# Kernel tuning notes

Hardware: AMD Instinct MI355X
Metric: run time of the kernel (lower is better)

## Reference

```python
import jax, jax.numpy as jnp
import numpy as np

VOCAB = 100000
EMBED = 64
SENT = 20
MEM = 50
BATCH = 32
HOPS = 3
PAD_ID = 0


def position_encoding(sentence_size, embedding_size):
    # Section 4.1 of MemN2N paper, vectorized. Returns [sentence_size, embedding_size].
    i = np.arange(1, embedding_size + 1, dtype=np.float32)[:, None]   # [E,1]
    j = np.arange(1, sentence_size + 1, dtype=np.float32)[None, :]    # [1,S]
    enc = (i - (embedding_size + 1) / 2.0) * (j - (sentence_size + 1) / 2.0)
    enc = 1.0 + 4.0 * enc / embedding_size / sentence_size
    enc[:, -1] = 1.0
    return jnp.asarray(enc.T, dtype=jnp.float32)  # [S,E]


def setup_inputs() -> dict:
    key = jax.random.key(0)
    k1, k2, k3, k4 = jax.random.split(key, 4)
    stories = jax.random.randint(k1, (BATCH, MEM, SENT), 0, VOCAB, dtype=jnp.int64 if jax.config.jax_enable_x64 else jnp.int32)
    queries = jax.random.randint(k2, (BATCH, SENT), 0, VOCAB, dtype=jnp.int64 if jax.config.jax_enable_x64 else jnp.int32)
    A = jax.random.normal(k3, (VOCAB, EMBED), dtype=jnp.float32) * 0.1
    C = jax.random.normal(k4, (HOPS, VOCAB, EMBED), dtype=jnp.float32) * 0.1
    # padding_idx=PAD_ID rows are zero, as in nn.Embedding(padding_idx=...)
    A = A.at[PAD_ID].set(0.0)
    C = C.at[:, PAD_ID].set(0.0)
    encoding = position_encoding(SENT, EMBED)
    return {"stories": stories, "queries": queries, "A": A, "C": C, "encoding": encoding}


def reference(stories, queries, A, C, encoding):
    # queries: [B,S], stories: [B,M,S], A: [V,E], C: [hops,V,E], encoding: [S,E]
    q_emb = A[queries]                                # [B,S,E]
    u = (q_emb * encoding).sum(axis=1)                # [B,E]
    for hop in range(HOPS):
        table_in = A if hop == 0 else C[hop - 1]
        emb_A = table_in[stories]                     # [B,M,S,E]
        m = (emb_A * encoding).sum(axis=2)            # [B,M,E]
        dotted = jnp.einsum('bme,be->bm', m, u)       # [B,M]
        probs = jax.nn.softmax(dotted, axis=-1)       # [B,M]
        emb_C = C[hop][stories]                       # [B,M,S,E]
        c = (emb_C * encoding).sum(axis=2)            # [B,M,E]
        o = jnp.einsum('bm,bme->be', probs, c)        # [B,E]
        u = u + o
    return u @ C[-1].T                                # [B,V]
```

## Files before the change

kernel.cpp:

```cpp
#include <hip/hip_runtime.h>
#include <hip/hip_bf16.h>

#define VOCAB 100000
#define EMBED 64
#define SENT  20
#define MEM   50
#define BATCH 32
#define HOPS  3

__device__ __forceinline__ float bfr(unsigned short x) {
    union { unsigned int u; float f; } cv;
    cv.u = ((unsigned int)x) << 16;
    return cv.f;
}

__device__ __forceinline__ bool is_bf16(const void* enc) {
    return ((const unsigned int*)enc)[639] == 0x3F803F80u;
}

__device__ __forceinline__ float loadT(const void* p, size_t idx, bool bf) {
    return bf ? bfr(((const unsigned short*)p)[idx]) : ((const float*)p)[idx];
}

__global__ void k_query(const int* __restrict__ queries,
                        const void* __restrict__ A,
                        const void* __restrict__ enc,
                        float* __restrict__ u)
{
    bool bf = is_bf16(enc);
    int b = blockIdx.x, e = threadIdx.x;
    int w = (e < SENT) ? queries[b * SENT + e] : 0;
    float acc = 0.f;
#pragma unroll
    for (int s = 0; s < SENT; ++s) {
        int ws = __shfl(w, s, 64);
        acc += loadT(A, (size_t)ws * EMBED + e, bf) * loadT(enc, s * EMBED + e, bf);
    }
    u[b * EMBED + e] = acc;
}

__global__ void k_hop1(const int* __restrict__ stories,
                       const void* __restrict__ Abase,
                       const void* __restrict__ Cbase,
                       size_t tin_off, size_t tc_off, int tin_is_A,
                       const void* __restrict__ enc,
                       const float* __restrict__ u,
                       float* __restrict__ c_ws,
                       float* __restrict__ dotted)
{
    bool bf = is_bf16(enc);
    const void* Tin = tin_is_A ? Abase : Cbase;
    size_t toff = tin_is_A ? 0 : tin_off;

    int bm = blockIdx.x;
    int b  = bm / MEM;
    int e  = threadIdx.x;
    int w  = (e < SENT) ? stories[bm * SENT + e] : 0;
    float macc = 0.f, cacc = 0.f;
#pragma unroll
    for (int s = 0; s < SENT; ++s) {
        int ws = __shfl(w, s, 64);
        float en = loadT(enc, s * EMBED + e, bf);
        macc += loadT(Tin,   toff  + (size_t)ws * EMBED + e, bf) * en;
        cacc += loadT(Cbase, tc_off + (size_t)ws * EMBED + e, bf) * en;
    }
    c_ws[bm * EMBED + e] = cacc;
    float d = macc * u[b * EMBED + e];
#pragma unroll
    for (int off = 32; off > 0; off >>= 1) d += __shfl_down(d, off, 64);
    if (e == 0) dotted[bm] = d;
}

__global__ void k_hop2(const float* __restrict__ dotted,
                       const float* __restrict__ c_ws,
                       float* __restrict__ u)
{
    int b = blockIdx.x, e = threadIdx.x;
    __shared__ float probs[MEM];
    float x = (e < MEM) ? dotted[b * MEM + e] : -3.4e38f;
    float mx = x;
#pragma unroll
    for (int off = 32; off > 0; off >>= 1) mx = fmaxf(mx, __shfl_xor(mx, off, 64));
    float ex = (e < MEM) ? __expf(x - mx) : 0.f;
    float sm = ex;
#pragma unroll
    for (int off = 32; off > 0; off >>= 1) sm += __shfl_xor(sm, off, 64);
    if (e < MEM) probs[e] = ex / sm;
    __syncthreads();
    float o = 0.f;
#pragma unroll
    for (int mm = 0; mm < MEM; ++mm)
        o += probs[mm] * c_ws[(b * MEM + mm) * EMBED + e];
    u[b * EMBED + e] += o;
}

__global__ __launch_bounds__(256) void k_out(const float* __restrict__ u,
                                             const void* __restrict__ Cbase,
                                             const void* __restrict__ enc,
                                             void* __restrict__ out)
{
    bool bf = is_bf16(enc);
    const size_t c2_off = (size_t)2 * VOCAB * EMBED;
    __shared__ __align__(16) float su[BATCH * EMBED];
    for (int i = threadIdx.x; i < BATCH * EMBED; i += 256) su[i] = u[i];
    __syncthreads();
    int v = blockIdx.x * 256 + threadIdx.x;
    if (v >= VOCAB) return;

    float row[EMBED];
    if (bf) {
        const uint4* rp = (const uint4*)((const unsigned short*)Cbase + c2_off + (size_t)v * EMBED);
#pragma unroll
        for (int i = 0; i < 8; ++i) {
            uint4 r = rp[i];
            row[i*8 + 0] = bfr((unsigned short)(r.x & 0xffff));
            row[i*8 + 1] = bfr((unsigned short)(r.x >> 16));
            row[i*8 + 2] = bfr((unsigned short)(r.y & 0xffff));
            row[i*8 + 3] = bfr((unsigned short)(r.y >> 16));
            row[i*8 + 4] = bfr((unsigned short)(r.z & 0xffff));
            row[i*8 + 5] = bfr((unsigned short)(r.z >> 16));
            row[i*8 + 6] = bfr((unsigned short)(r.w & 0xffff));
            row[i*8 + 7] = bfr((unsigned short)(r.w >> 16));
        }
    } else {
        const float4* rp = (const float4*)((const float*)Cbase + c2_off + (size_t)v * EMBED);
#pragma unroll
        for (int i = 0; i < 16; ++i) {
            float4 r = rp[i];
            row[i*4 + 0] = r.x; row[i*4 + 1] = r.y;
            row[i*4 + 2] = r.z; row[i*4 + 3] = r.w;
        }
    }

    float res[BATCH];
#pragma unroll
    for (int b = 0; b < BATCH; ++b) {
        const float4* sp = (const float4*)(su + b * EMBED);
        float acc = 0.f;
#pragma unroll
        for (int e4 = 0; e4 < 16; ++e4) {
            float4 us = sp[e4];
            acc += row[e4*4+0]*us.x + row[e4*4+1]*us.y
                 + row[e4*4+2]*us.z + row[e4*4+3]*us.w;
        }
        res[b] = acc;
    }

    if (bf) {
        unsigned short* ob = (unsigned short*)out;
#pragma unroll
        for (int b = 0; b < BATCH; ++b) {
            __hip_bfloat16 h = __float2bfloat16(res[b]);
            ob[(size_t)b * VOCAB + v] = *(unsigned short*)&h;
        }
    } else {
        float* of = (float*)out;
#pragma unroll
        for (int b = 0; b < BATCH; ++b)
            of[(size_t)b * VOCAB + v] = res[b];
    }
}

extern "C" void kernel_launch(void* const* d_in, const int* in_sizes, int n_in,
                              void* d_out, int out_size, void* d_ws, size_t ws_size,
                              hipStream_t stream)
{
    const int*  stories = (const int*)d_in[0];
    const int*  queries = (const int*)d_in[1];
    const void* A       = d_in[2];
    const void* C       = d_in[3];
    const void* enc     = d_in[4];

    float* u      = (float*)d_ws;
    float* c_ws   = u + BATCH * EMBED;
    float* dotted = c_ws + BATCH * MEM * EMBED;

    k_query<<<BATCH, 64, 0, stream>>>(queries, A, enc, u);

    for (int hop = 0; hop < HOPS; ++hop) {
        size_t tin_off = (size_t)(hop - 1) * VOCAB * EMBED;
        size_t tc_off  = (size_t)hop * VOCAB * EMBED;
        k_hop1<<<BATCH * MEM, 64, 0, stream>>>(stories, A, C,
                                               tin_off, tc_off, hop == 0 ? 1 : 0,
                                               enc, u, c_ws, dotted);
        k_hop2<<<BATCH, 64, 0, stream>>>(dotted, c_ws, u);
    }

    k_out<<<(VOCAB + 255) / 256, 256, 0, stream>>>(u, C, enc, d_out);
}
```

Baseline: 166.3 us.

## Fuse query embedding and all memory hops into one per-batch kernel

Replaces the query kernel and the three hop1/hop2 kernel pairs with a single kernel that runs one 1024-thread block per batch row. Sixteen waves each gather and encode memory slots into LDS, then compute the softmax and the weighted sum in-block, keeping u in registers across hops. This removes six kernel launches and the global-memory round trips for c, dotted and u. The cost is that only 32 blocks run on the GPU, so the gather latency is hidden by fewer waves than in the old 1600-block hop kernel.

```diff
diff --git a/kernel.cpp b/kernel.cpp
--- a/kernel.cpp
+++ b/kernel.cpp
@@ -22,76 +22,82 @@
     return bf ? bfr(((const unsigned short*)p)[idx]) : ((const float*)p)[idx];
 }
 
-__global__ void k_query(const int* __restrict__ queries,
-                        const void* __restrict__ A,
-                        const void* __restrict__ enc,
-                        float* __restrict__ u)
-{
-    bool bf = is_bf16(enc);
-    int b = blockIdx.x, e = threadIdx.x;
-    int w = (e < SENT) ? queries[b * SENT + e] : 0;
-    float acc = 0.f;
+__device__ __forceinline__ float wave_sum(float d) {
 #pragma unroll
-    for (int s = 0; s < SENT; ++s) {
-        int ws = __shfl(w, s, 64);
-        acc += loadT(A, (size_t)ws * EMBED + e, bf) * loadT(enc, s * EMBED + e, bf);
-    }
-    u[b * EMBED + e] = acc;
+    for (int off = 32; off > 0; off >>= 1) d += __shfl_xor(d, off, 64);
+    return d;
 }
 
-__global__ void k_hop1(const int* __restrict__ stories,
-                       const void* __restrict__ Abase,
-                       const void* __restrict__ Cbase,
-                       size_t tin_off, size_t tc_off, int tin_is_A,
-                       const void* __restrict__ enc,
-                       const float* __restrict__ u,
-                       float* __restrict__ c_ws,
-                       float* __restrict__ dotted)
+__global__ __launch_bounds__(1024) void k_recur(
+    const int* __restrict__ stories,
+    const int* __restrict__ queries,
+    const void* __restrict__ A,
+    const void* __restrict__ C,
+    const void* __restrict__ enc,
+    float* __restrict__ u3g)
 {
-    bool bf = is_bf16(enc);
-    const void* Tin = tin_is_A ? Abase : Cbase;
-    size_t toff = tin_is_A ? 0 : tin_off;
+    const bool bf = is_bf16(enc);
+    const int b    = blockIdx.x;
+    const int tid  = threadIdx.x;
+    const int e    = tid & 63;
+    const int widx = tid >> 6;
 
-    int bm = blockIdx.x;
-    int b  = bm / MEM;
-    int e  = threadIdx.x;
-    int w  = (e < SENT) ? stories[bm * SENT + e] : 0;
-    float macc = 0.f, cacc = 0.f;
+    __shared__ float cls[MEM][EMBED];
+    __shared__ float dls[MEM];
+
+    const size_t VE = (size_t)VOCAB * EMBED;
+
+    float encr[SENT];
 #pragma unroll
-    for (int s = 0; s < SENT; ++s) {
-        int ws = __shfl(w, s, 64);
-        float en = loadT(enc, s * EMBED + e, bf);
-        macc += loadT(Tin,   toff  + (size_t)ws * EMBED + e, bf) * en;
-        cacc += loadT(Cbase, tc_off + (size_t)ws * EMBED + e, bf) * en;
+    for (int s = 0; s < SENT; ++s) encr[s] = loadT(enc, s * EMBED + e, bf);
+
+    float u_e = 0.f;
+    {
+        int wq = (e < SENT) ? queries[b * SENT + e] : 0;
+#pragma unroll
+        for (int s = 0; s < SENT; ++s) {
+            int w = __shfl(wq, s, 64);
+            u_e += loadT(A, (size_t)w * EMBED + e, bf) * encr[s];
+        }
     }
-    c_ws[bm * EMBED + e] = cacc;
-    float d = macc * u[b * EMBED + e];
+
+    for (int hop = 0; hop < HOPS; ++hop) {
+        const void* Tin   = (hop == 0) ? A : C;
+        const size_t toff = (hop == 2) ? VE : 0;
+        const size_t coff = (size_t)hop * VE;
+
+        for (int mm = widx; mm < MEM; mm += 16) {
+            int wst = (e < SENT) ? stories[(b * MEM + mm) * SENT + e] : 0;
+            float macc = 0.f, cacc = 0.f;
 #pragma unroll
-    for (int off = 32; off > 0; off >>= 1) d += __shfl_down(d, off, 64);
-    if (e == 0) dotted[bm] = d;
-}
+            for (int s = 0; s < SENT; ++s) {
+                int w = __shfl(wst, s, 64);
+                size_t ro = (size_t)w * EMBED + e;
+                macc += loadT(Tin, toff + ro, bf) * encr[s];
+                cacc += loadT(C, coff + ro, bf) * encr[s];
+            }
+            cls[mm][e] = cacc;
+            float d = wave_sum(macc * u_e);
+            if (e == 0) dls[mm] = d;
+        }
+        __syncthreads();
 
-__global__ void k_hop2(const float* __restrict__ dotted,
-                       const float* __restrict__ c_ws,
-                       float* __restrict__ u)
-{
-    int b = blockIdx.x, e = threadIdx.x;
-    __shared__ float probs[MEM];
-    float x = (e < MEM) ? dotted[b * MEM + e] : -3.4e38f;
-    float mx = x;
+        float x = (e < MEM) ? dls[e] : -3.4e38f;
+        float mx = x;
 #pragma unroll
-    for (int off = 32; off > 0; off >>= 1) mx = fmaxf(mx, __shfl_xor(mx, off, 64));
-    float ex = (e < MEM) ? __expf(x - mx) : 0.f;
-    float sm = ex;
+        for (int off = 32; off > 0; off >>= 1) mx = fmaxf(mx, __shfl_xor(mx, off, 64));
+        float ex = (e < MEM) ? __expf(x - mx) : 0.f;
+        float sm = wave_sum(ex);
+        float p = ex / sm;
+        float o = 0.f;
 #pragma unroll
-    for (int off = 32; off > 0; off >>= 1) sm += __shfl_xor(sm, off, 64);
-    if (e < MEM) probs[e] = ex / sm;
-    __syncthreads();
-    float o = 0.f;
-#pragma unroll
-    for (int mm = 0; mm < MEM; ++mm)
-        o += probs[mm] * c_ws[(b * MEM + mm) * EMBED + e];
-    u[b * EMBED + e] += o;
+        for (int mm = 0; mm < MEM; ++mm)
+            o += __shfl(p, mm, 64) * cls[mm][e];
+        u_e += o;
+        __syncthreads();
+    }
+
+    if (widx == 0) u3g[b * EMBED + e] = u_e;
 }
 
 __global__ __launch_bounds__(256) void k_out(const float* __restrict__ u,
@@ -134,8 +140,8 @@
 
     float res[BATCH];
 #pragma unroll
-    for (int b = 0; b < BATCH; ++b) {
-        const float4* sp = (const float4*)(su + b * EMBED);
+    for (int bb = 0; bb < BATCH; ++bb) {
+        const float4* sp = (const float4*)(su + bb * EMBED);
         float acc = 0.f;
 #pragma unroll
         for (int e4 = 0; e4 < 16; ++e4) {
@@ -143,21 +149,21 @@
             acc += row[e4*4+0]*us.x + row[e4*4+1]*us.y
                  + row[e4*4+2]*us.z + row[e4*4+3]*us.w;
         }
-        res[b] = acc;
+        res[bb] = acc;
     }
 
     if (bf) {
         unsigned short* ob = (unsigned short*)out;
 #pragma unroll
-        for (int b = 0; b < BATCH; ++b) {
-            __hip_bfloat16 h = __float2bfloat16(res[b]);
-            ob[(size_t)b * VOCAB + v] = *(unsigned short*)&h;
+        for (int bb = 0; bb < BATCH; ++bb) {
+            __hip_bfloat16 h = __float2bfloat16(res[bb]);
+            ob[(size_t)bb * VOCAB + v] = *(unsigned short*)&h;
         }
     } else {
         float* of = (float*)out;
 #pragma unroll
-        for (int b = 0; b < BATCH; ++b)
-            of[(size_t)b * VOCAB + v] = res[b];
+        for (int bb = 0; bb < BATCH; ++bb)
+            of[(size_t)bb * VOCAB + v] = res[bb];
     }
 }
 
@@ -170,21 +176,8 @@
     const void* A       = d_in[2];
     const void* C       = d_in[3];
     const void* enc     = d_in[4];
+    float*      u3g     = (float*)d_ws;
 
-    float* u      = (float*)d_ws;
-    float* c_ws   = u + BATCH * EMBED;
-    float* dotted = c_ws + BATCH * MEM * EMBED;
-
-    k_query<<<BATCH, 64, 0, stream>>>(queries, A, enc, u);
-
-    for (int hop = 0; hop < HOPS; ++hop) {
-        size_t tin_off = (size_t)(hop - 1) * VOCAB * EMBED;
-        size_t tc_off  = (size_t)hop * VOCAB * EMBED;
-        k_hop1<<<BATCH * MEM, 64, 0, stream>>>(stories, A, C,
-                                               tin_off, tc_off, hop == 0 ? 1 : 0,
-                                               enc, u, c_ws, dotted);
-        k_hop2<<<BATCH, 64, 0, stream>>>(dotted, c_ws, u);
-    }
-
-    k_out<<<(VOCAB + 255) / 256, 256, 0, stream>>>(u, C, enc, d_out);
+    k_recur<<<BATCH, 1024, 0, stream>>>(stories, queries, A, C, enc, u3g);
+    k_out<<<(VOCAB + 255) / 256, 256, 0, stream>>>(u3g, C, enc, d_out);
 }
```

Result: slower. 192.7 us (+15.9%).
